# Optimization experiments

Hardware: AMD Instinct MI355X
Metric: run time of the kernel (lower is better)

## Reference

```python
import jax, jax.numpy as jnp
import numpy as np

N_AP, N_UE, D = 256, 1024, 64  # dimension = 64 in source

def setup_inputs() -> dict:
    key = jax.random.key(0)
    ks = jax.random.split(key, 9)
    s = 1.0 / np.sqrt(2 * D)
    return {
        "ap_hid": jax.random.normal(ks[0], (N_AP, D), jnp.float32),
        "ue_hid": jax.random.normal(ks[1], (N_UE, D), jnp.float32),
        "edge_hid": jax.random.normal(ks[2], (N_AP, N_UE, D), jnp.float32),
        "W1": jax.random.normal(ks[3], (2 * D, D), jnp.float32) * s,
        "b1": jnp.zeros((D,), jnp.float32),
        "W2": jax.random.normal(ks[4], (2 * D, D), jnp.float32) * s,
        "b2": jnp.zeros((D,), jnp.float32),
        "W3": jax.random.normal(ks[5], (2 * D, D), jnp.float32) * s,
        "b3": jnp.zeros((D,), jnp.float32),
    }

def reference(ap_hid, ue_hid, edge_hid, W1, b1, W2, b2, W3, b3):
    # edge_hid[a, u] is the feature of edge (AP a, UE u); eid is (a, u) itself.
    A, U, d = edge_hid.shape

    # reduce_func_ap: per-AP mailbox over all UE neighbors -> mlp1(cat(ap_hid, edge_hid))
    ap_in = jnp.concatenate(
        [jnp.broadcast_to(ap_hid[:, None, :], (A, U, d)), edge_hid], axis=-1)  # [A,U,2d]
    ap_res = jax.nn.relu(jnp.einsum('auk,kd->aud', ap_in, W1) + b1)            # [A,U,d]

    # reduce_func_ue: per-UE mailbox over all AP neighbors -> mlp2(cat(ue_hid, edge_hid))
    edge_ua = jnp.swapaxes(edge_hid, 0, 1)                                     # [U,A,d]
    ue_in = jnp.concatenate(
        [jnp.broadcast_to(ue_hid[:, None, :], (U, A, d)), edge_ua], axis=-1)   # [U,A,2d]
    ue_res = jax.nn.relu(jnp.einsum('uak,kd->uad', ue_in, W2) + b2)            # [U,A,d]

    # message_func_edge: for edge (a,u), sum src AP's ap_result excluding the
    # mailbox slot whose eid matches this edge, plus same for dst UE's ue_result.
    ap_sum = ap_res.sum(axis=1)   # [A,d]
    ue_sum = ue_res.sum(axis=1)   # [U,d]
    agg = (ap_sum[:, None, :] - ap_res) \
        + (ue_sum[None, :, :] - jnp.swapaxes(ue_res, 0, 1))                     # [A,U,d]

    new = jnp.einsum('auk,kd->aud', jnp.concatenate([edge_hid, agg], axis=-1), W3) + b3
    return new  # new edge 'hid' for both AP2UE and UE2AP, shape [A,U,d]
```

## Files before the change

kernel.cpp:

```cpp
#include <hip/hip_runtime.h>


#define A_N 256
#define U_N 1024

typedef short short8 __attribute__((ext_vector_type(8)));
typedef float f32x4 __attribute__((ext_vector_type(4)));

__device__ __forceinline__ unsigned short f2bf(float f) {
  unsigned int u = __float_as_uint(f);
  return (unsigned short)((u + 0x7FFFu + ((u >> 16) & 1u)) >> 16);
}

__device__ __forceinline__ f32x4 mfma16(short8 a, short8 b, f32x4 c) {
  return __builtin_amdgcn_mfma_f32_16x16x32_bf16(a, b, c, 0, 0, 0);
}

__device__ __forceinline__ void cvt16(const float4& e0, const float4& e1,
                                      const float4& e2, const float4& e3,
                                      short8& a0, short8& a1) {
  a0[0] = (short)f2bf(e0.x); a0[1] = (short)f2bf(e0.y);
  a0[2] = (short)f2bf(e0.z); a0[3] = (short)f2bf(e0.w);
  a0[4] = (short)f2bf(e1.x); a0[5] = (short)f2bf(e1.y);
  a0[6] = (short)f2bf(e1.z); a0[7] = (short)f2bf(e1.w);
  a1[0] = (short)f2bf(e2.x); a1[1] = (short)f2bf(e2.y);
  a1[2] = (short)f2bf(e2.z); a1[3] = (short)f2bf(e2.w);
  a1[4] = (short)f2bf(e3.x); a1[5] = (short)f2bf(e3.y);
  a1[6] = (short)f2bf(e3.z); a1[7] = (short)f2bf(e3.w);
}

__device__ __forceinline__ void rowmlp_row(const float* __restrict__ in,
                                           const float* __restrict__ W,
                                           const float* __restrict__ bias,
                                           float* __restrict__ out, int r, int lane) {
  float rv = in[r * 64 + lane];
  float acc = bias ? bias[lane] : 0.f;
#pragma unroll
  for (int k = 0; k < 64; k++) acc += __shfl(rv, k, 64) * W[k * 64 + lane];
  out[r * 64 + lane] = acc;
}

__global__ __launch_bounds__(256) void k_prep(
    const float* __restrict__ ap_hid, const float* __restrict__ ue_hid,
    const float* __restrict__ W1, const float* __restrict__ b1,
    const float* __restrict__ W2, const float* __restrict__ b2,
    const float* __restrict__ W3, unsigned short* __restrict__ Wt,
    float* __restrict__ c1, float* __restrict__ c2) {
  int bx = blockIdx.x, tid = threadIdx.x;
  if (bx < 64) {
    int idx = bx * 256 + tid;
    int r = idx >> 6, k = idx & 63;
    int sec = r >> 6, d = r & 63;
    float v;
    if (sec == 0)      v = W1[(64 + k) * 64 + d];
    else if (sec == 1) v = W2[(64 + k) * 64 + d];
    else if (sec == 2) v = W3[k * 64 + d];
    else               v = W3[(64 + k) * 64 + d];
    Wt[r * 64 + k] = f2bf(v);
  } else if (bx < 128) {
    int r = (bx - 64) * 4 + (tid >> 6);
    rowmlp_row(ap_hid, W1, b1, c1, r, tid & 63);
  } else {
    int r = (bx - 128) * 4 + (tid >> 6);
    rowmlp_row(ue_hid, W2, b2, c2, r, tid & 63);
  }
}

__global__ __launch_bounds__(256) void k_pass1(
    const float* __restrict__ edge, const unsigned short* __restrict__ Wt,
    const float* __restrict__ c1, const float* __restrict__ c2,
    float* __restrict__ ap_part, float* __restrict__ ue_part) {
  __shared__ float ap_l[4 * 64];
  int tid = threadIdx.x, lane = tid & 63, w = tid >> 6;
  int fr = lane & 15, fq = lane >> 4;
  int chunk = blockIdx.x >> 4;
  int panel = blockIdx.x & 15;
  int a0 = chunk * 4;
  int u0 = panel * 64;
  int urow = u0 + w * 16 + fr;
  const float* erow = edge + urow * 64 + fq * 8;

  ap_l[tid] = 0.f;
  __syncthreads();

  short8 bw[8][2];
#pragma unroll
  for (int nt = 0; nt < 8; nt++)
#pragma unroll
    for (int ks = 0; ks < 2; ks++)
      bw[nt][ks] = *(const short8*)(Wt + (nt * 16 + fr) * 64 + ks * 32 + fq * 8);

  float c2v[4][4];
#pragma unroll
  for (int j = 0; j < 4; j++)
#pragma unroll
    for (int i = 0; i < 4; i++)
      c2v[j][i] = c2[(u0 + w * 16 + fq * 4 + i) * 64 + j * 16 + fr];

  float ureg[4][4];
#pragma unroll
  for (int j = 0; j < 4; j++)
#pragma unroll
    for (int i = 0; i < 4; i++) ureg[j][i] = 0.f;

  const float* p0 = erow + a0 * 65536;
  float4 e0 = *(const float4*)(p0);
  float4 e1 = *(const float4*)(p0 + 4);
  float4 e2 = *(const float4*)(p0 + 32);
  float4 e3 = *(const float4*)(p0 + 36);
  float c1v[4];
#pragma unroll
  for (int j = 0; j < 4; j++) c1v[j] = c1[a0 * 64 + j * 16 + fr];

  for (int c = 0; c < 4; c++) {
    int a = a0 + c;
    float4 n0, n1, n2, n3;
    float nc1[4];
    if (c < 3) {
      const float* np = erow + (a + 1) * 65536;
      n0 = *(const float4*)(np);
      n1 = *(const float4*)(np + 4);
      n2 = *(const float4*)(np + 32);
      n3 = *(const float4*)(np + 36);
#pragma unroll
      for (int j = 0; j < 4; j++) nc1[j] = c1[(a + 1) * 64 + j * 16 + fr];
    }
    short8 af0, af1;
    cvt16(e0, e1, e2, e3, af0, af1);

#pragma unroll
    for (int j = 0; j < 4; j++) {
      f32x4 acc = {0.f, 0.f, 0.f, 0.f};
      acc = mfma16(af0, bw[j][0], acc);
      acc = mfma16(af1, bw[j][1], acc);
      float cv = c1v[j];
      float rs = fmaxf(acc[0] + cv, 0.f) + fmaxf(acc[1] + cv, 0.f) +
                 fmaxf(acc[2] + cv, 0.f) + fmaxf(acc[3] + cv, 0.f);
      rs += __shfl_xor(rs, 16, 64);
      rs += __shfl_xor(rs, 32, 64);
      if (lane < 16) atomicAdd(&ap_l[c * 64 + j * 16 + lane], rs);
    }
#pragma unroll
    for (int j = 0; j < 4; j++) {
      f32x4 acc = {0.f, 0.f, 0.f, 0.f};
      acc = mfma16(af0, bw[4 + j][0], acc);
      acc = mfma16(af1, bw[4 + j][1], acc);
#pragma unroll
      for (int i = 0; i < 4; i++)
        ureg[j][i] += fmaxf(acc[i] + c2v[j][i], 0.f);
    }
    if (c < 3) {
      e0 = n0; e1 = n1; e2 = n2; e3 = n3;
#pragma unroll
      for (int j = 0; j < 4; j++) c1v[j] = nc1[j];
    }
  }
#pragma unroll
  for (int j = 0; j < 4; j++)
#pragma unroll
    for (int i = 0; i < 4; i++)
      ue_part[(chunk * 1024 + u0 + w * 16 + fq * 4 + i) * 64 + j * 16 + fr] =
          ureg[j][i];
  __syncthreads();
  ap_part[(panel * 256 + a0 + w) * 64 + lane] = ap_l[tid];
}

__global__ __launch_bounds__(256) void k_mid(
    const float* __restrict__ ap_part, const float* __restrict__ ue_part,
    const float* __restrict__ W3, const float* __restrict__ b3,
    float* __restrict__ s3, float* __restrict__ s4) {
  __shared__ float red[4][64];
  int bx = blockIdx.x, tid = threadIdx.x, lane = tid & 63, w = tid >> 6;
  const float* W3b = W3 + 4096;
  if (bx < 64) {
    int r = bx * 4 + w;
    float v = 0.f;
#pragma unroll
    for (int p = 0; p < 16; p++) v += ap_part[(p * 256 + r) * 64 + lane];
    float acc = 0.f;
#pragma unroll
    for (int k = 0; k < 64; k++) acc += __shfl(v, k, 64) * W3b[k * 64 + lane];
    s3[r * 64 + lane] = acc;
  } else {
    int r = bx - 64;
    float v = 0.f;
#pragma unroll
    for (int q = 0; q < 16; q++)
      v += ue_part[((w * 16 + q) * 1024 + r) * 64 + lane];
    red[w][lane] = v;
    __syncthreads();
    if (w == 0) {
      float vv = red[0][lane] + red[1][lane] + red[2][lane] + red[3][lane];
      float acc = b3[lane];
#pragma unroll
      for (int k = 0; k < 64; k++) acc += __shfl(vv, k, 64) * W3b[k * 64 + lane];
      s4[r * 64 + lane] = acc;
    }
  }
}

__global__ __launch_bounds__(256) void k_pass2(
    const float* __restrict__ edge, const unsigned short* __restrict__ Wt,
    const float* __restrict__ c1, const float* __restrict__ c2,
    const float* __restrict__ s3, const float* __restrict__ s4,
    float* __restrict__ out) {
  __shared__ unsigned short W_lds[128 * 72];
  __shared__ unsigned short t_lds[64 * 72];
  int tid = threadIdx.x, lane = tid & 63, w = tid >> 6;
  int fr = lane & 15, fq = lane >> 4;
  int a = blockIdx.x >> 2;
  int ubase = (blockIdx.x & 3) * 256;

#pragma unroll
  for (int it = 0; it < 4; it++) {
    int r = it * 32 + (tid >> 3), seg = tid & 7;
    *(uint4*)&W_lds[r * 72 + seg * 8] = *(const uint4*)(Wt + r * 64 + seg * 8);
  }

  short8 w3t[4][2], w3b[4][2];
#pragma unroll
  for (int j = 0; j < 4; j++)
#pragma unroll
    for (int ks = 0; ks < 2; ks++) {
      w3t[j][ks] = *(const short8*)(Wt + (128 + j * 16 + fr) * 64 + ks * 32 + fq * 8);
      w3b[j][ks] = *(const short8*)(Wt + (192 + j * 16 + fr) * 64 + ks * 32 + fq * 8);
    }

  float c1v[4], s3v[4];
#pragma unroll
  for (int j = 0; j < 4; j++) {
    c1v[j] = c1[a * 64 + j * 16 + fr];
    s3v[j] = s3[a * 64 + j * 16 + fr];
  }

  const float* er0 = edge + (a * 1024 + ubase + w * 16 + fr) * 64 + fq * 8;
  float4 e0 = *(const float4*)(er0);
  float4 e1 = *(const float4*)(er0 + 4);
  float4 e2 = *(const float4*)(er0 + 32);
  float4 e3 = *(const float4*)(er0 + 36);
  float c2v[4][4], s4v[4][4];
#pragma unroll
  for (int j = 0; j < 4; j++)
#pragma unroll
    for (int i = 0; i < 4; i++) {
      int u = ubase + w * 16 + fq * 4 + i;
      c2v[j][i] = c2[u * 64 + j * 16 + fr];
      s4v[j][i] = s4[u * 64 + j * 16 + fr];
    }

  __syncthreads();

  for (int pnl = 0; pnl < 4; pnl++) {
    int upan = ubase + pnl * 64;
    float4 n0, n1, n2, n3;
    float c2n[4][4], s4n[4][4];
    if (pnl < 3) {
      const float* nr = edge + (a * 1024 + upan + 64 + w * 16 + fr) * 64 + fq * 8;
      n0 = *(const float4*)(nr);
      n1 = *(const float4*)(nr + 4);
      n2 = *(const float4*)(nr + 32);
      n3 = *(const float4*)(nr + 36);
#pragma unroll
      for (int j = 0; j < 4; j++)
#pragma unroll
        for (int i = 0; i < 4; i++) {
          int u = upan + 64 + w * 16 + fq * 4 + i;
          c2n[j][i] = c2[u * 64 + j * 16 + fr];
          s4n[j][i] = s4[u * 64 + j * 16 + fr];
        }
    }
    short8 af0, af1;
    cvt16(e0, e1, e2, e3, af0, af1);

    f32x4 accP3[4];
#pragma unroll
    for (int j = 0; j < 4; j++) {
      const unsigned short* wr = &W_lds[(j * 16 + fr) * 72 + fq * 8];
      short8 b10 = *(const short8*)(wr);
      short8 b11 = *(const short8*)(wr + 32);
      short8 b20 = *(const short8*)(wr + 64 * 72);
      short8 b21 = *(const short8*)(wr + 64 * 72 + 32);
      f32x4 a1 = {0.f, 0.f, 0.f, 0.f};
      a1 = mfma16(af0, b10, a1);
      a1 = mfma16(af1, b11, a1);
      f32x4 a2 = {0.f, 0.f, 0.f, 0.f};
      a2 = mfma16(af0, b20, a2);
      a2 = mfma16(af1, b21, a2);
      f32x4 p3 = {0.f, 0.f, 0.f, 0.f};
      p3 = mfma16(af0, w3t[j][0], p3);
      p3 = mfma16(af1, w3t[j][1], p3);
      accP3[j] = p3;
#pragma unroll
      for (int i = 0; i < 4; i++) {
        float tv = fmaxf(a1[i] + c1v[j], 0.f) + fmaxf(a2[i] + c2v[j][i], 0.f);
        t_lds[(w * 16 + fq * 4 + i) * 72 + j * 16 + fr] = f2bf(tv);
      }
    }
    short8 tf0 = *(const short8*)&t_lds[(w * 16 + fr) * 72 + fq * 8];
    short8 tf1 = *(const short8*)&t_lds[(w * 16 + fr) * 72 + 32 + fq * 8];
#pragma unroll
    for (int j = 0; j < 4; j++) {
      f32x4 acc = {0.f, 0.f, 0.f, 0.f};
      acc = mfma16(tf0, w3b[j][0], acc);
      acc = mfma16(tf1, w3b[j][1], acc);
#pragma unroll
      for (int i = 0; i < 4; i++) {
        int u = upan + w * 16 + fq * 4 + i;
        out[(a * 1024 + u) * 64 + j * 16 + fr] =
            accP3[j][i] - acc[i] + s3v[j] + s4v[j][i];
      }
    }
    if (pnl < 3) {
      e0 = n0; e1 = n1; e2 = n2; e3 = n3;
#pragma unroll
      for (int j = 0; j < 4; j++)
#pragma unroll
        for (int i = 0; i < 4; i++) {
          c2v[j][i] = c2n[j][i];
          s4v[j][i] = s4n[j][i];
        }
    }
  }
}

extern "C" void kernel_launch(void* const* d_in, const int* in_sizes, int n_in,
                              void* d_out, int out_size, void* d_ws, size_t ws_size,
                              hipStream_t stream) {
  const float* ap_hid = (const float*)d_in[0];
  const float* ue_hid = (const float*)d_in[1];
  const float* edge   = (const float*)d_in[2];
  const float* W1     = (const float*)d_in[3];
  const float* b1     = (const float*)d_in[4];
  const float* W2     = (const float*)d_in[5];
  const float* b2     = (const float*)d_in[6];
  const float* W3     = (const float*)d_in[7];
  const float* b3     = (const float*)d_in[8];
  float* out = (float*)d_out;

  char* ws = (char*)d_ws;
  unsigned short* Wt = (unsigned short*)ws;
  float* c1      = (float*)(ws + 32768);
  float* c2      = (float*)(ws + 98304);
  float* s3      = (float*)(ws + 360448);
  float* s4      = (float*)(ws + 425984);
  float* ap_part = (float*)(ws + 688128);
  float* ue_part = (float*)(ws + 4882432);

  k_prep<<<384, 256, 0, stream>>>(ap_hid, ue_hid, W1, b1, W2, b2, W3, Wt, c1, c2);
  k_pass1<<<1024, 256, 0, stream>>>(edge, Wt, c1, c2, ap_part, ue_part);
  k_mid<<<1088, 256, 0, stream>>>(ap_part, ue_part, W3, b3, s3, s4);
  k_pass2<<<1024, 256, 0, stream>>>(edge, Wt, c1, c2, s3, s4, out);
}
```

Before: 171.5 us.

## Stage edge tiles via async global-to-LDS loads with swizzle in both passes

Both edge-streaming kernels now issue asynchronous global_load_lds transfers into a triple-buffered, XOR-swizzled LDS staging area, with explicit vmcnt waits, instead of prefetching float4s into registers. The goal is to keep more edge bytes in flight per wave and cut register pressure so memory latency stays hidden. Separately, k_mid gives each wave a whole UE row (64 partials) with no shared-memory reduction or barrier, and launches fewer blocks. The risks are more LDS per block, which may lower occupancy, and hand-tuned waitcnt values that must match the real instruction count.

Result: slower. 175.2 us (+2.2%).

```diff
diff --git a/kernel.cpp b/kernel.cpp
--- a/kernel.cpp
+++ b/kernel.cpp
@@ -6,6 +6,9 @@
 
 typedef short short8 __attribute__((ext_vector_type(8)));
 typedef float f32x4 __attribute__((ext_vector_type(4)));
+
+#define WAITVM(N) asm volatile("s_waitcnt vmcnt(" #N ")" ::: "memory")
+#define WAITLGKM0 asm volatile("s_waitcnt lgkmcnt(0)" ::: "memory")
 
 __device__ __forceinline__ unsigned short f2bf(float f) {
   unsigned int u = __float_as_uint(f);
@@ -14,6 +17,32 @@
 
 __device__ __forceinline__ f32x4 mfma16(short8 a, short8 b, f32x4 c) {
   return __builtin_amdgcn_mfma_f32_16x16x32_bf16(a, b, c, 0, 0, 0);
+}
+
+__device__ __forceinline__ void gload16(const void* g, void* l) {
+  __builtin_amdgcn_global_load_lds(
+      (const __attribute__((address_space(1))) void*)g,
+      (__attribute__((address_space(3))) void*)l, 16, 0, 0);
+}
+
+__device__ __forceinline__ void stage_tile(const char* gtile, char* ltile, int lane) {
+#pragma unroll
+  for (int k = 0; k < 4; k++) {
+    int loff = k * 1024 + lane * 16;
+    int sw = ((k * 4 + (lane >> 4)) & 7) << 4;
+    gload16(gtile + (loff ^ sw), ltile + k * 1024);
+  }
+}
+
+__device__ __forceinline__ void read_tile(const char* ltile, int fr, int fq,
+                                          float4& e0, float4& e1,
+                                          float4& e2, float4& e3) {
+  int sw = (fr & 7) << 4;
+  const char* rb = ltile + fr * 256;
+  e0 = *(const float4*)(rb + ((fq * 32 + 0) ^ sw));
+  e1 = *(const float4*)(rb + ((fq * 32 + 16) ^ sw));
+  e2 = *(const float4*)(rb + ((fq * 32 + 128) ^ sw));
+  e3 = *(const float4*)(rb + ((fq * 32 + 144) ^ sw));
 }
 
 __device__ __forceinline__ void cvt16(const float4& e0, const float4& e1,
@@ -71,18 +100,23 @@
     const float* __restrict__ c1, const float* __restrict__ c2,
     float* __restrict__ ap_part, float* __restrict__ ue_part) {
   __shared__ float ap_l[4 * 64];
+  __shared__ __align__(16) char estage[49152];
   int tid = threadIdx.x, lane = tid & 63, w = tid >> 6;
   int fr = lane & 15, fq = lane >> 4;
   int chunk = blockIdx.x >> 4;
   int panel = blockIdx.x & 15;
   int a0 = chunk * 4;
   int u0 = panel * 64;
-  int urow = u0 + w * 16 + fr;
-  const float* erow = edge + urow * 64 + fq * 8;
 
   ap_l[tid] = 0.f;
   __syncthreads();
 
+  const char* gwave = (const char*)(edge + (size_t)(u0 + w * 16) * 64);
+  char* lwave = estage + w * 4096;
+  stage_tile(gwave + (size_t)(a0 + 0) * 262144, lwave, lane);
+  stage_tile(gwave + (size_t)(a0 + 1) * 262144, lwave + 16384, lane);
+  stage_tile(gwave + (size_t)(a0 + 2) * 262144, lwave + 32768, lane);
+
   short8 bw[8][2];
 #pragma unroll
   for (int nt = 0; nt < 8; nt++)
@@ -103,27 +137,26 @@
 #pragma unroll
     for (int i = 0; i < 4; i++) ureg[j][i] = 0.f;
 
-  const float* p0 = erow + a0 * 65536;
-  float4 e0 = *(const float4*)(p0);
-  float4 e1 = *(const float4*)(p0 + 4);
-  float4 e2 = *(const float4*)(p0 + 32);
-  float4 e3 = *(const float4*)(p0 + 36);
   float c1v[4];
 #pragma unroll
   for (int j = 0; j < 4; j++) c1v[j] = c1[a0 * 64 + j * 16 + fr];
 
+#pragma unroll
   for (int c = 0; c < 4; c++) {
-    int a = a0 + c;
-    float4 n0, n1, n2, n3;
+    if (c == 0)      { WAITVM(8); }
+    else if (c == 1) { WAITVM(8); }
+    else if (c == 2) { WAITVM(8); }
+    else             { WAITVM(4); }
+    float4 e0, e1, e2, e3;
+    read_tile(lwave + (c % 3) * 16384, fr, fq, e0, e1, e2, e3);
+    if (c == 0) {
+      WAITLGKM0;
+      stage_tile(gwave + (size_t)(a0 + 3) * 262144, lwave, lane);
+    }
     float nc1[4];
     if (c < 3) {
-      const float* np = erow + (a + 1) * 65536;
-      n0 = *(const float4*)(np);
-      n1 = *(const float4*)(np + 4);
-      n2 = *(const float4*)(np + 32);
-      n3 = *(const float4*)(np + 36);
-#pragma unroll
-      for (int j = 0; j < 4; j++) nc1[j] = c1[(a + 1) * 64 + j * 16 + fr];
+#pragma unroll
+      for (int j = 0; j < 4; j++) nc1[j] = c1[(a0 + c + 1) * 64 + j * 16 + fr];
     }
     short8 af0, af1;
     cvt16(e0, e1, e2, e3, af0, af1);
@@ -150,7 +183,6 @@
         ureg[j][i] += fmaxf(acc[i] + c2v[j][i], 0.f);
     }
     if (c < 3) {
-      e0 = n0; e1 = n1; e2 = n2; e3 = n3;
 #pragma unroll
       for (int j = 0; j < 4; j++) c1v[j] = nc1[j];
     }
@@ -169,11 +201,10 @@
     const float* __restrict__ ap_part, const float* __restrict__ ue_part,
     const float* __restrict__ W3, const float* __restrict__ b3,
     float* __restrict__ s3, float* __restrict__ s4) {
-  __shared__ float red[4][64];
-  int bx = blockIdx.x, tid = threadIdx.x, lane = tid & 63, w = tid >> 6;
+  int bx = blockIdx.x, tid = threadIdx.x, lane = tid & 63;
   const float* W3b = W3 + 4096;
   if (bx < 64) {
-    int r = bx * 4 + w;
+    int r = bx * 4 + (tid >> 6);
     float v = 0.f;
 #pragma unroll
     for (int p = 0; p < 16; p++) v += ap_part[(p * 256 + r) * 64 + lane];
@@ -182,20 +213,14 @@
     for (int k = 0; k < 64; k++) acc += __shfl(v, k, 64) * W3b[k * 64 + lane];
     s3[r * 64 + lane] = acc;
   } else {
-    int r = bx - 64;
+    int r = (bx - 64) * 4 + (tid >> 6);
     float v = 0.f;
 #pragma unroll
-    for (int q = 0; q < 16; q++)
-      v += ue_part[((w * 16 + q) * 1024 + r) * 64 + lane];
-    red[w][lane] = v;
-    __syncthreads();
-    if (w == 0) {
-      float vv = red[0][lane] + red[1][lane] + red[2][lane] + red[3][lane];
-      float acc = b3[lane];
-#pragma unroll
-      for (int k = 0; k < 64; k++) acc += __shfl(vv, k, 64) * W3b[k * 64 + lane];
-      s4[r * 64 + lane] = acc;
-    }
+    for (int p = 0; p < 64; p++) v += ue_part[(p * 1024 + r) * 64 + lane];
+    float acc = b3[lane];
+#pragma unroll
+    for (int k = 0; k < 64; k++) acc += __shfl(v, k, 64) * W3b[k * 64 + lane];
+    s4[r * 64 + lane] = acc;
   }
 }
 
@@ -206,6 +231,7 @@
     float* __restrict__ out) {
   __shared__ unsigned short W_lds[128 * 72];
   __shared__ unsigned short t_lds[64 * 72];
+  __shared__ __align__(16) char estage[49152];
   int tid = threadIdx.x, lane = tid & 63, w = tid >> 6;
   int fr = lane & 15, fq = lane >> 4;
   int a = blockIdx.x >> 2;
@@ -216,28 +242,6 @@
     int r = it * 32 + (tid >> 3), seg = tid & 7;
     *(uint4*)&W_lds[r * 72 + seg * 8] = *(const uint4*)(Wt + r * 64 + seg * 8);
   }
-
-  short8 w3t[4][2], w3b[4][2];
-#pragma unroll
-  for (int j = 0; j < 4; j++)
-#pragma unroll
-    for (int ks = 0; ks < 2; ks++) {
-      w3t[j][ks] = *(const short8*)(Wt + (128 + j * 16 + fr) * 64 + ks * 32 + fq * 8);
-      w3b[j][ks] = *(const short8*)(Wt + (192 + j * 16 + fr) * 64 + ks * 32 + fq * 8);
-    }
-
-  float c1v[4], s3v[4];
-#pragma unroll
-  for (int j = 0; j < 4; j++) {
-    c1v[j] = c1[a * 64 + j * 16 + fr];
-    s3v[j] = s3[a * 64 + j * 16 + fr];
-  }
-
-  const float* er0 = edge + (a * 1024 + ubase + w * 16 + fr) * 64 + fq * 8;
-  float4 e0 = *(const float4*)(er0);
-  float4 e1 = *(const float4*)(er0 + 4);
-  float4 e2 = *(const float4*)(er0 + 32);
-  float4 e3 = *(const float4*)(er0 + 36);
   float c2v[4][4], s4v[4][4];
 #pragma unroll
   for (int j = 0; j < 4; j++)
@@ -247,19 +251,44 @@
       c2v[j][i] = c2[u * 64 + j * 16 + fr];
       s4v[j][i] = s4[u * 64 + j * 16 + fr];
     }
+  short8 w3t[4][2], w3b[4][2];
+#pragma unroll
+  for (int j = 0; j < 4; j++)
+#pragma unroll
+    for (int ks = 0; ks < 2; ks++) {
+      w3t[j][ks] = *(const short8*)(Wt + (128 + j * 16 + fr) * 64 + ks * 32 + fq * 8);
+      w3b[j][ks] = *(const short8*)(Wt + (192 + j * 16 + fr) * 64 + ks * 32 + fq * 8);
+    }
+  float c1v[4], s3v[4];
+#pragma unroll
+  for (int j = 0; j < 4; j++) {
+    c1v[j] = c1[a * 64 + j * 16 + fr];
+    s3v[j] = s3[a * 64 + j * 16 + fr];
+  }
 
   __syncthreads();
 
+  const char* gwave = (const char*)(edge + (size_t)(a * 1024 + ubase + w * 16) * 64);
+  char* lwave = estage + w * 4096;
+  stage_tile(gwave + 0,     lwave, lane);
+  stage_tile(gwave + 16384, lwave + 16384, lane);
+  stage_tile(gwave + 32768, lwave + 32768, lane);
+
+#pragma unroll
   for (int pnl = 0; pnl < 4; pnl++) {
+    if (pnl == 0)      { WAITVM(8); }
+    else if (pnl == 1) { WAITVM(40); }
+    else if (pnl == 2) { WAITVM(40); }
+    else               { WAITVM(32); }
+    float4 e0, e1, e2, e3;
+    read_tile(lwave + (pnl % 3) * 16384, fr, fq, e0, e1, e2, e3);
+    if (pnl == 0) {
+      WAITLGKM0;
+      stage_tile(gwave + 49152, lwave, lane);
+    }
     int upan = ubase + pnl * 64;
-    float4 n0, n1, n2, n3;
     float c2n[4][4], s4n[4][4];
     if (pnl < 3) {
-      const float* nr = edge + (a * 1024 + upan + 64 + w * 16 + fr) * 64 + fq * 8;
-      n0 = *(const float4*)(nr);
-      n1 = *(const float4*)(nr + 4);
-      n2 = *(const float4*)(nr + 32);
-      n3 = *(const float4*)(nr + 36);
 #pragma unroll
       for (int j = 0; j < 4; j++)
 #pragma unroll
@@ -311,7 +340,6 @@
       }
     }
     if (pnl < 3) {
-      e0 = n0; e1 = n1; e2 = n2; e3 = n3;
 #pragma unroll
       for (int j = 0; j < 4; j++)
 #pragma unroll
@@ -348,6 +376,6 @@
 
   k_prep<<<384, 256, 0, stream>>>(ap_hid, ue_hid, W1, b1, W2, b2, W3, Wt, c1, c2);
   k_pass1<<<1024, 256, 0, stream>>>(edge, Wt, c1, c2, ap_part, ue_part);
-  k_mid<<<1088, 256, 0, stream>>>(ap_part, ue_part, W3, b3, s3, s4);
+  k_mid<<<320, 256, 0, stream>>>(ap_part, ue_part, W3, b3, s3, s4);
   k_pass2<<<1024, 256, 0, stream>>>(edge, Wt, c1, c2, s3, s4, out);
 }
```
